# Performance work log

Measured on AMD Instinct MI355X. Metric: run time of the kernel, lower is better.

The kernel has to match this reference:

```python
import jax, jax.numpy as jnp
import numpy as np

H = 16      # num_attention_heads
D = 64      # head_dim
W = 256     # one-sided attention window (tokens attend to +/- W neighbors)


def setup_inputs() -> dict:
    key = jax.random.key(0)
    ks = jax.random.split(key, 7)
    B, S, E = 2, 4096, 1024
    init = lambda k, shape: jax.random.normal(k, shape, jnp.float32) * 0.02
    return {
        "hidden_states": jax.random.normal(ks[0], (B, S, E), jnp.float32),
        "Wq": init(ks[1], (E, E)), "bq": init(ks[2], (E,)),
        "Wk": init(ks[3], (E, E)), "bk": init(ks[4], (E,)),
        "Wv": init(ks[5], (E, E)), "bv": init(ks[6], (E,)),
    }


def _sliding_window_attn(q, k, v, S):
    """q,k,v: [B,H,S,D]. Banded attention: query i attends keys |i-j|<=W.
    Implemented via overlapping chunks (sliding_chunks style), never forming SxS."""
    B = q.shape[0]
    C = S // W  # number of query chunks
    qc = q.reshape(B, H, C, W, D)

    def window(x):
        # pad one chunk each side, then stack 3 consecutive chunks per query chunk
        xp = jnp.pad(x, ((0, 0), (0, 0), (W, W), (0, 0)))
        xr = xp.reshape(B, H, C + 2, W, D)
        return jnp.concatenate([xr[:, :, i:i + C] for i in range(3)], axis=3)  # [B,H,C,3W,D]

    kc, vc = window(k), window(v)

    i = jnp.arange(W)[:, None]            # query offset within chunk
    j = jnp.arange(3 * W)[None, :]        # key offset within 3W window
    band = jnp.abs(j - W - i) <= W        # [W,3W] band mask
    kpos = jnp.arange(C)[:, None, None] * W + (j - W)[None]  # absolute key pos [C,1,3W]
    valid = band[None] & (kpos >= 0) & (kpos < S)             # [C,W,3W]

    scores = jnp.einsum('bhcqd,bhckd->bhcqk', qc, kc)         # [B,H,C,W,3W]
    scores = jnp.where(valid[None, None], scores, -jnp.inf)
    probs = jax.nn.softmax(scores, axis=-1)
    out = jnp.einsum('bhcqk,bhckd->bhcqd', probs, vc)         # [B,H,C,W,D]
    return out.reshape(B, H, S, D)


def reference(hidden_states, Wq, bq, Wk, bk, Wv, bv):
    B, S, E = hidden_states.shape
    scale = 1.0 / np.sqrt(D).astype(np.float32)

    def split_heads(x):  # [B,S,E] -> [B,H,S,D]
        return x.reshape(B, S, H, D).transpose(0, 2, 1, 3)

    q = split_heads((hidden_states @ Wq.T + bq) * scale)
    k = split_heads(hidden_states @ Wk.T + bk)
    v = split_heads(hidden_states @ Wv.T + bv)

    ctx = _sliding_window_attn(q, k, v, S)                 # [B,H,S,D]
    return ctx.transpose(0, 2, 1, 3).reshape(B, S, E)      # [B,S,E]
```

## Files before the change

kernel.cpp:

```cpp
#include <hip/hip_runtime.h>

#define NH 16
#define HD 64
#define WIN 256
#define BB 2
#define SS 4096
#define EE 1024

typedef __attribute__((ext_vector_type(8))) short short8;
typedef __attribute__((ext_vector_type(4))) float floatx4;
typedef __attribute__((ext_vector_type(4))) unsigned short ushort4v;

__device__ inline unsigned short f2bf(float f) {
    unsigned u = __builtin_bit_cast(unsigned, f);
    u += 0x7fffu + ((u >> 16) & 1u);
    return (unsigned short)(u >> 16);
}

__global__ __launch_bounds__(256)
void cvt_kernel(const float* __restrict__ X,
                const float* __restrict__ W0,
                const float* __restrict__ W1,
                const float* __restrict__ W2,
                unsigned short* __restrict__ out)
{
    size_t idx = (size_t)blockIdx.x * 256 + threadIdx.x;
    const size_t X4 = 2097152, W4 = 262144;
    const float* src; unsigned short* dst; size_t off;
    if (idx < X4)                { src = X;  dst = out;            off = idx; }
    else if (idx < X4 + W4)      { src = W0; dst = out + 8388608;  off = idx - X4; }
    else if (idx < X4 + 2 * W4)  { src = W1; dst = out + 9437184;  off = idx - X4 - W4; }
    else                         { src = W2; dst = out + 10485760; off = idx - X4 - 2 * W4; }
    float4 v = ((const float4*)src)[off];
    ushort4 u;
    u.x = f2bf(v.x); u.y = f2bf(v.y); u.z = f2bf(v.z); u.w = f2bf(v.w);
    ((ushort4*)dst)[off] = u;
}

__global__ __launch_bounds__(256, 4)
void qkv_gemm4(const unsigned short* __restrict__ Xb,
               const unsigned short* __restrict__ WbAll,
               const float* __restrict__ b0,
               const float* __restrict__ b1,
               const float* __restrict__ b2,
               unsigned short* __restrict__ Qo,
               unsigned short* __restrict__ Ko,
               unsigned short* __restrict__ Vo)
{
    const int id = blockIdx.x;
    const int xcd = id & 7;
    const int rest = id >> 3;
    const int ytile = xcd + 8 * (rest & 7);
    const int nm = rest >> 3;
    const int ntile = nm & 7;
    const int mode = nm >> 3;

    const unsigned short* Wm = WbAll + (size_t)mode * 1048576;
    const float* bm = (mode == 0) ? b0 : (mode == 1) ? b1 : b2;
    unsigned short* outp = (mode == 0) ? Qo : (mode == 1) ? Ko : Vo;

    const int m0 = ytile * 128;
    const int n0 = ntile * 128;
    const int t = threadIdx.x;
    const int lane = t & 63;
    const int wv = t >> 6;
    const int wm = wv >> 1, wn = wv & 1;
    const int lg = lane >> 4, lc = lane & 15;

    __shared__ __attribute__((aligned(16))) unsigned short smem[16384];
    unsigned short* As[2] = { smem, smem + 4096 };
    unsigned short* Bs[2] = { smem + 8192, smem + 12288 };

    const int srow = lane >> 2;
    const int scol = (lane & 3) * 8;

    floatx4 acc[4][4];
#pragma unroll
    for (int i = 0; i < 4; ++i)
#pragma unroll
        for (int j = 0; j < 4; ++j)
            acc[i][j] = (floatx4)0.0f;

    for (int kt = 0; kt < EE; kt += 64) {
        if (kt) __syncthreads();
#pragma unroll
        for (int half = 0; half < 2; ++half) {
#pragma unroll
            for (int seg = 0; seg < 2; ++seg) {
                int r0 = wv * 32 + seg * 16;
                const unsigned short* asrc =
                    Xb + (size_t)(m0 + r0 + srow) * EE + kt + half * 32 + scol;
                const unsigned short* bsrc =
                    Wm + (size_t)(n0 + r0 + srow) * EE + kt + half * 32 + scol;
                __builtin_amdgcn_global_load_lds(
                    (const __attribute__((address_space(1))) unsigned int*)asrc,
                    (__attribute__((address_space(3))) unsigned int*)&As[half][r0 * 32], 16, 0, 0);
                __builtin_amdgcn_global_load_lds(
                    (const __attribute__((address_space(1))) unsigned int*)bsrc,
                    (__attribute__((address_space(3))) unsigned int*)&Bs[half][r0 * 32], 16, 0, 0);
            }
        }
        __syncthreads();

#pragma unroll
        for (int half = 0; half < 2; ++half) {
            short8 af[4], bfr[4];
#pragma unroll
            for (int mt = 0; mt < 4; ++mt)
                af[mt] = *(const short8*)(&As[half][(wm * 64 + mt * 16 + lc) * 32 + lg * 8]);
#pragma unroll
            for (int nt = 0; nt < 4; ++nt)
                bfr[nt] = *(const short8*)(&Bs[half][(wn * 64 + nt * 16 + lc) * 32 + lg * 8]);
#pragma unroll
            for (int mt = 0; mt < 4; ++mt)
#pragma unroll
                for (int nt = 0; nt < 4; ++nt)
                    acc[mt][nt] = __builtin_amdgcn_mfma_f32_16x16x32_bf16(
                        af[mt], bfr[nt], acc[mt][nt], 0, 0, 0);
        }
    }

    const int CST = 136;
    const float qscale = (mode == 0) ? 0.125f : 1.0f;
#pragma unroll
    for (int p = 0; p < 2; ++p) {
        __syncthreads();
        if (mode < 2) {
            if (wm == p) {
#pragma unroll
                for (int nt = 0; nt < 4; ++nt) {
                    float bias = bm[n0 + wn * 64 + nt * 16 + lc];
#pragma unroll
                    for (int mt = 0; mt < 4; ++mt)
#pragma unroll
                        for (int r = 0; r < 4; ++r) {
                            int ml = mt * 16 + lg * 4 + r;
                            int nl = wn * 64 + nt * 16 + lc;
                            smem[ml * CST + nl] = f2bf((acc[mt][nt][r] + bias) * qscale);
                        }
                }
            }
        } else {
            if (wn == p) {
#pragma unroll
                for (int nt = 0; nt < 4; ++nt) {
                    float bias = bm[n0 + p * 64 + nt * 16 + lc];
#pragma unroll
                    for (int mt = 0; mt < 4; ++mt) {
                        ushort4v pk;
#pragma unroll
                        for (int r = 0; r < 4; ++r)
                            pk[r] = f2bf(acc[mt][nt][r] + bias);
                        int nl = nt * 16 + lc;
                        int col = wm * 64 + mt * 16 + lg * 4;
                        *(ushort4v*)(&smem[nl * CST + col]) = pk;
                    }
                }
            }
        }
        __syncthreads();
#pragma unroll
        for (int q = 0; q < 4; ++q) {
            int c = q * 256 + t;
            int row = c >> 4;
            int j = c & 15;
            uint4 val = *(const uint4*)(&smem[row * CST + j * 8]);
            if (mode < 2) {
                int m = m0 + p * 64 + row;
                int bb = m >> 12, s = m & (SS - 1);
                int n = n0 + j * 8;
                int hh = n >> 6, dd = n & 63;
                *(uint4*)(outp + (((size_t)bb * NH + hh) * SS + s) * HD + dd) = val;
            } else {
                int n = n0 + p * 64 + row;
                int hh = n >> 6, dd = n & 63;
                int m = m0 + j * 8;
                int bb = m >> 12, s = m & (SS - 1);
                *(uint4*)(outp + (((size_t)bb * NH + hh) * HD + dd) * SS + s) = val;
            }
        }
    }
}

__global__ __launch_bounds__(256, 2)
void swa_kernel(const unsigned short* __restrict__ Qp_,
                const unsigned short* __restrict__ Kp_,
                const unsigned short* __restrict__ Vp_,
                float* __restrict__ outp)
{
    const int id = blockIdx.x;
    const int xcd = id & 7;
    const int idx = id >> 3;
    const int bh = xcd + 8 * (idx >> 5);
    const int q0 = (idx & 31) * 128;
    const int b = bh >> 4;
    const int h = bh & 15;
    const int t = threadIdx.x, lane = t & 63, wv = t >> 6;
    const int lg = lane >> 4, lc = lane & 15;
    const size_t bhs = (size_t)b * NH + h;
    const unsigned short* Qp = Qp_ + bhs * (size_t)SS * HD;
    const unsigned short* Kp = Kp_ + bhs * (size_t)SS * HD;
    const unsigned short* Vp = Vp_ + bhs * (size_t)HD * SS;
    const int qbase = q0 + wv * 32;

    short8 qf[2][2];
#pragma unroll
    for (int rt = 0; rt < 2; ++rt)
#pragma unroll
        for (int hh = 0; hh < 2; ++hh)
            qf[rt][hh] = *(const short8*)(Qp + (size_t)(qbase + rt * 16 + lc) * HD + hh * 32 + lg * 8);

    floatx4 o[2][4];
    float lsum[2][4];
#pragma unroll
    for (int rt = 0; rt < 2; ++rt)
#pragma unroll
        for (int i = 0; i < 4; ++i) { o[rt][i] = (floatx4)0.0f; lsum[rt][i] = 0.0f; }

    __shared__ __attribute__((aligned(16))) unsigned short kvs[2][2][4096];
    __shared__ __attribute__((aligned(16))) unsigned short Ps[4][2][16][72];

    const int kbeg = (q0 >= WIN) ? (q0 - WIN) : 0;
    const int kend = (q0 + 128 + WIN <= SS) ? (q0 + 128 + WIN) : SS;

    const int sr = lane >> 3;
    const int sj = lane & 7;
    const int swz = (sj ^ sr) * 8;

#define STAGE(buf, k0_)                                                              \
    {                                                                                \
        _Pragma("unroll")                                                            \
        for (int i = 0; i < 2; ++i) {                                                \
            int rbase = 16 * wv + i * 8;                                             \
            const unsigned short* ks = Kp + (size_t)((k0_) + rbase + sr) * HD + swz; \
            const unsigned short* vs = Vp + (size_t)(rbase + sr) * SS + (k0_) + swz; \
            __builtin_amdgcn_global_load_lds(                                        \
                (const __attribute__((address_space(1))) unsigned int*)ks,           \
                (__attribute__((address_space(3))) unsigned int*)&kvs[buf][0][rbase * 64], 16, 0, 0); \
            __builtin_amdgcn_global_load_lds(                                        \
                (const __attribute__((address_space(1))) unsigned int*)vs,           \
                (__attribute__((address_space(3))) unsigned int*)&kvs[buf][1][rbase * 64], 16, 0, 0); \
        }                                                                            \
    }

    STAGE(0, kbeg)

    int cur = 0;
    for (int k0 = kbeg; k0 < kend; k0 += 64, cur ^= 1) {
        __syncthreads();
        bool active = (k0 + 63 >= qbase - WIN) && (k0 <= qbase + 31 + WIN);
        short8 kc[4][2], vf[4][2];
        if (active) {
#pragma unroll
            for (int nt = 0; nt < 4; ++nt)
#pragma unroll
                for (int hh = 0; hh < 2; ++hh) {
                    int row = nt * 16 + lc;
                    kc[nt][hh] = *(const short8*)(&kvs[cur][0][row * 64 + (((hh * 4 + lg) ^ (row & 7)) * 8)]);
                    vf[nt][hh] = *(const short8*)(&kvs[cur][1][row * 64 + (((hh * 4 + lg) ^ (row & 7)) * 8)]);
                }
        }
        if (k0 + 64 < kend) STAGE(cur ^ 1, k0 + 64)
        if (!active) continue;

        bool fullband = (k0 >= qbase - 225) && (k0 <= qbase + 193);

        floatx4 sc[2][4];
#pragma unroll
        for (int rt = 0; rt < 2; ++rt)
#pragma unroll
            for (int nt = 0; nt < 4; ++nt) {
                floatx4 z = (floatx4)0.0f;
                z = __builtin_amdgcn_mfma_f32_16x16x32_bf16(qf[rt][0], kc[nt][0], z, 0, 0, 0);
                sc[rt][nt] = __builtin_amdgcn_mfma_f32_16x16x32_bf16(qf[rt][1], kc[nt][1], z, 0, 0, 0);
            }
#pragma unroll
        for (int rt = 0; rt < 2; ++rt)
#pragma unroll
            for (int nt = 0; nt < 4; ++nt)
#pragma unroll
                for (int r = 0; r < 4; ++r)
                    sc[rt][nt][r] = __expf(sc[rt][nt][r]);
        if (!fullband) {
#pragma unroll
            for (int rt = 0; rt < 2; ++rt)
#pragma unroll
                for (int nt = 0; nt < 4; ++nt) {
                    int kk = k0 + nt * 16 + lc;
#pragma unroll
                    for (int r = 0; r < 4; ++r) {
                        int dq = (qbase + rt * 16 + lg * 4 + r) - kk;
                        if (dq > WIN || dq < -WIN) sc[rt][nt][r] = 0.0f;
                    }
                }
        }
#pragma unroll
        for (int rt = 0; rt < 2; ++rt)
#pragma unroll
            for (int r = 0; r < 4; ++r)
                lsum[rt][r] += (sc[rt][0][r] + sc[rt][1][r]) + (sc[rt][2][r] + sc[rt][3][r]);
#pragma unroll
        for (int rt = 0; rt < 2; ++rt)
#pragma unroll
            for (int nt = 0; nt < 4; ++nt)
#pragma unroll
                for (int r = 0; r < 4; ++r)
                    Ps[wv][rt][lg * 4 + r][nt * 16 + lc] = f2bf(sc[rt][nt][r]);
#pragma unroll
        for (int rt = 0; rt < 2; ++rt) {
            short8 pa0 = *(const short8*)(&Ps[wv][rt][lc][lg * 8]);
            short8 pa1 = *(const short8*)(&Ps[wv][rt][lc][32 + lg * 8]);
#pragma unroll
            for (int nt2 = 0; nt2 < 4; ++nt2) {
                o[rt][nt2] = __builtin_amdgcn_mfma_f32_16x16x32_bf16(pa0, vf[nt2][0], o[rt][nt2], 0, 0, 0);
                o[rt][nt2] = __builtin_amdgcn_mfma_f32_16x16x32_bf16(pa1, vf[nt2][1], o[rt][nt2], 0, 0, 0);
            }
        }
    }

#pragma unroll
    for (int rt = 0; rt < 2; ++rt)
#pragma unroll
        for (int r = 0; r < 4; ++r) {
            float rs = lsum[rt][r];
#pragma unroll
            for (int off = 1; off < 16; off <<= 1)
                rs += __shfl_xor(rs, off, 64);
            lsum[rt][r] = 1.0f / rs;
        }
#pragma unroll
    for (int rt = 0; rt < 2; ++rt)
#pragma unroll
        for (int nt2 = 0; nt2 < 4; ++nt2)
#pragma unroll
            for (int r = 0; r < 4; ++r) {
                int q = qbase + rt * 16 + lg * 4 + r;
                int d = nt2 * 16 + lc;
                outp[((size_t)b * SS + q) * EE + h * HD + d] = o[rt][nt2][r] * lsum[rt][r];
            }
}

extern "C" void kernel_launch(void* const* d_in, const int* in_sizes, int n_in,
                              void* d_out, int out_size, void* d_ws, size_t ws_size,
                              hipStream_t stream) {
    const float* X  = (const float*)d_in[0];
    const float* Wq = (const float*)d_in[1];
    const float* bq = (const float*)d_in[2];
    const float* Wk = (const float*)d_in[3];
    const float* bk = (const float*)d_in[4];
    const float* Wv = (const float*)d_in[5];
    const float* bv = (const float*)d_in[6];

    const size_t qkv_elems = (size_t)BB * NH * SS * HD;
    unsigned short* Qw = (unsigned short*)d_ws;
    unsigned short* Kw = Qw + qkv_elems;
    unsigned short* Vw = Kw + qkv_elems;

    unsigned short* cvt = (unsigned short*)d_out;
    const unsigned short* Xb = cvt;
    const unsigned short* WbAll = cvt + 8388608;

    cvt_kernel<<<dim3(11264), 256, 0, stream>>>(X, Wq, Wk, Wv, cvt);
    qkv_gemm4<<<dim3(1536), 256, 0, stream>>>(
        Xb, WbAll, bq, bk, bv, Qw, Kw, Vw);
    swa_kernel<<<dim3(1024), 256, 0, stream>>>(Qw, Kw, Vw, (float*)d_out);
}
```

Baseline: 193.5 us.

## Split attention work across 8 waves of 16 query rows each

```diff
diff --git a/kernel.cpp b/kernel.cpp
--- a/kernel.cpp
+++ b/kernel.cpp
@@ -182,7 +182,7 @@
     }
 }
 
-__global__ __launch_bounds__(256, 2)
+__global__ __launch_bounds__(512, 4)
 void swa_kernel(const unsigned short* __restrict__ Qp_,
                 const unsigned short* __restrict__ Kp_,
                 const unsigned short* __restrict__ Vp_,
@@ -201,24 +201,20 @@
     const unsigned short* Qp = Qp_ + bhs * (size_t)SS * HD;
     const unsigned short* Kp = Kp_ + bhs * (size_t)SS * HD;
     const unsigned short* Vp = Vp_ + bhs * (size_t)HD * SS;
-    const int qbase = q0 + wv * 32;
-
-    short8 qf[2][2];
-#pragma unroll
-    for (int rt = 0; rt < 2; ++rt)
-#pragma unroll
-        for (int hh = 0; hh < 2; ++hh)
-            qf[rt][hh] = *(const short8*)(Qp + (size_t)(qbase + rt * 16 + lc) * HD + hh * 32 + lg * 8);
-
-    floatx4 o[2][4];
-    float lsum[2][4];
-#pragma unroll
-    for (int rt = 0; rt < 2; ++rt)
-#pragma unroll
-        for (int i = 0; i < 4; ++i) { o[rt][i] = (floatx4)0.0f; lsum[rt][i] = 0.0f; }
+    const int qbase = q0 + wv * 16;
+
+    short8 qf[2];
+#pragma unroll
+    for (int hh = 0; hh < 2; ++hh)
+        qf[hh] = *(const short8*)(Qp + (size_t)(qbase + lc) * HD + hh * 32 + lg * 8);
+
+    floatx4 o[4];
+    float lsum[4];
+#pragma unroll
+    for (int i = 0; i < 4; ++i) { o[i] = (floatx4)0.0f; lsum[i] = 0.0f; }
 
     __shared__ __attribute__((aligned(16))) unsigned short kvs[2][2][4096];
-    __shared__ __attribute__((aligned(16))) unsigned short Ps[4][2][16][72];
+    __shared__ __attribute__((aligned(16))) unsigned short Ps[8][16][72];
 
     const int kbeg = (q0 >= WIN) ? (q0 - WIN) : 0;
     const int kend = (q0 + 128 + WIN <= SS) ? (q0 + 128 + WIN) : SS;
@@ -229,18 +225,15 @@
 
 #define STAGE(buf, k0_)                                                              \
     {                                                                                \
-        _Pragma("unroll")                                                            \
-        for (int i = 0; i < 2; ++i) {                                                \
-            int rbase = 16 * wv + i * 8;                                             \
-            const unsigned short* ks = Kp + (size_t)((k0_) + rbase + sr) * HD + swz; \
-            const unsigned short* vs = Vp + (size_t)(rbase + sr) * SS + (k0_) + swz; \
-            __builtin_amdgcn_global_load_lds(                                        \
-                (const __attribute__((address_space(1))) unsigned int*)ks,           \
-                (__attribute__((address_space(3))) unsigned int*)&kvs[buf][0][rbase * 64], 16, 0, 0); \
-            __builtin_amdgcn_global_load_lds(                                        \
-                (const __attribute__((address_space(1))) unsigned int*)vs,           \
-                (__attribute__((address_space(3))) unsigned int*)&kvs[buf][1][rbase * 64], 16, 0, 0); \
-        }                                                                            \
+        const int rbase = 8 * wv;                                                    \
+        const unsigned short* ks = Kp + (size_t)((k0_) + rbase + sr) * HD + swz;     \
+        const unsigned short* vs = Vp + (size_t)(rbase + sr) * SS + (k0_) + swz;     \
+        __builtin_amdgcn_global_load_lds(                                            \
+            (const __attribute__((address_space(1))) unsigned int*)ks,               \
+            (__attribute__((address_space(3))) unsigned int*)&kvs[buf][0][rbase * 64], 16, 0, 0); \
+        __builtin_amdgcn_global_load_lds(                                            \
+            (const __attribute__((address_space(1))) unsigned int*)vs,               \
+            (__attribute__((address_space(3))) unsigned int*)&kvs[buf][1][rbase * 64], 16, 0, 0); \
     }
 
     STAGE(0, kbeg)
@@ -248,8 +241,8 @@
     int cur = 0;
     for (int k0 = kbeg; k0 < kend; k0 += 64, cur ^= 1) {
         __syncthreads();
-        bool active = (k0 + 63 >= qbase - WIN) && (k0 <= qbase + 31 + WIN);
-        short8 kc[4][2], vf[4][2];
+        bool active = (k0 + 63 >= qbase - WIN) && (k0 <= qbase + 15 + WIN);
+        short8 kc[4][2];
         if (active) {
 #pragma unroll
             for (int nt = 0; nt < 4; ++nt)
@@ -257,87 +250,73 @@
                 for (int hh = 0; hh < 2; ++hh) {
                     int row = nt * 16 + lc;
                     kc[nt][hh] = *(const short8*)(&kvs[cur][0][row * 64 + (((hh * 4 + lg) ^ (row & 7)) * 8)]);
-                    vf[nt][hh] = *(const short8*)(&kvs[cur][1][row * 64 + (((hh * 4 + lg) ^ (row & 7)) * 8)]);
                 }
         }
         if (k0 + 64 < kend) STAGE(cur ^ 1, k0 + 64)
         if (!active) continue;
 
-        bool fullband = (k0 >= qbase - 225) && (k0 <= qbase + 193);
-
-        floatx4 sc[2][4];
-#pragma unroll
-        for (int rt = 0; rt < 2; ++rt)
+        bool fullband = (k0 >= qbase - 241) && (k0 <= qbase + 193);
+
+        floatx4 sc[4];
+#pragma unroll
+        for (int nt = 0; nt < 4; ++nt) {
+            floatx4 z = (floatx4)0.0f;
+            z = __builtin_amdgcn_mfma_f32_16x16x32_bf16(qf[0], kc[nt][0], z, 0, 0, 0);
+            sc[nt] = __builtin_amdgcn_mfma_f32_16x16x32_bf16(qf[1], kc[nt][1], z, 0, 0, 0);
+        }
+#pragma unroll
+        for (int nt = 0; nt < 4; ++nt)
+#pragma unroll
+            for (int r = 0; r < 4; ++r)
+                sc[nt][r] = __expf(sc[nt][r]);
+        if (!fullband) {
 #pragma unroll
             for (int nt = 0; nt < 4; ++nt) {
-                floatx4 z = (floatx4)0.0f;
-                z = __builtin_amdgcn_mfma_f32_16x16x32_bf16(qf[rt][0], kc[nt][0], z, 0, 0, 0);
-                sc[rt][nt] = __builtin_amdgcn_mfma_f32_16x16x32_bf16(qf[rt][1], kc[nt][1], z, 0, 0, 0);
-            }
-#pragma unroll
-        for (int rt = 0; rt < 2; ++rt)
-#pragma unroll
-            for (int nt = 0; nt < 4; ++nt)
-#pragma unroll
-                for (int r = 0; r < 4; ++r)
-                    sc[rt][nt][r] = __expf(sc[rt][nt][r]);
-        if (!fullband) {
-#pragma unroll
-            for (int rt = 0; rt < 2; ++rt)
-#pragma unroll
-                for (int nt = 0; nt < 4; ++nt) {
-                    int kk = k0 + nt * 16 + lc;
-#pragma unroll
-                    for (int r = 0; r < 4; ++r) {
-                        int dq = (qbase + rt * 16 + lg * 4 + r) - kk;
-                        if (dq > WIN || dq < -WIN) sc[rt][nt][r] = 0.0f;
-                    }
+                int kk = k0 + nt * 16 + lc;
+#pragma unroll
+                for (int r = 0; r < 4; ++r) {
+                    int dq = (qbase + lg * 4 + r) - kk;
+                    if (dq > WIN || dq < -WIN) sc[nt][r] = 0.0f;
                 }
-        }
-#pragma unroll
-        for (int rt = 0; rt < 2; ++rt)
+            }
+        }
+#pragma unroll
+        for (int r = 0; r < 4; ++r)
+            lsum[r] += (sc[0][r] + sc[1][r]) + (sc[2][r] + sc[3][r]);
+#pragma unroll
+        for (int nt = 0; nt < 4; ++nt)
 #pragma unroll
             for (int r = 0; r < 4; ++r)
-                lsum[rt][r] += (sc[rt][0][r] + sc[rt][1][r]) + (sc[rt][2][r] + sc[rt][3][r]);
-#pragma unroll
-        for (int rt = 0; rt < 2; ++rt)
-#pragma unroll
-            for (int nt = 0; nt < 4; ++nt)
-#pragma unroll
-                for (int r = 0; r < 4; ++r)
-                    Ps[wv][rt][lg * 4 + r][nt * 16 + lc] = f2bf(sc[rt][nt][r]);
-#pragma unroll
-        for (int rt = 0; rt < 2; ++rt) {
-            short8 pa0 = *(const short8*)(&Ps[wv][rt][lc][lg * 8]);
-            short8 pa1 = *(const short8*)(&Ps[wv][rt][lc][32 + lg * 8]);
-#pragma unroll
-            for (int nt2 = 0; nt2 < 4; ++nt2) {
-                o[rt][nt2] = __builtin_amdgcn_mfma_f32_16x16x32_bf16(pa0, vf[nt2][0], o[rt][nt2], 0, 0, 0);
-                o[rt][nt2] = __builtin_amdgcn_mfma_f32_16x16x32_bf16(pa1, vf[nt2][1], o[rt][nt2], 0, 0, 0);
-            }
-        }
-    }
-
-#pragma unroll
-    for (int rt = 0; rt < 2; ++rt)
+                Ps[wv][lg * 4 + r][nt * 16 + lc] = f2bf(sc[nt][r]);
+
+        short8 pa0 = *(const short8*)(&Ps[wv][lc][lg * 8]);
+        short8 pa1 = *(const short8*)(&Ps[wv][lc][32 + lg * 8]);
+#pragma unroll
+        for (int nt2 = 0; nt2 < 4; ++nt2) {
+            int row = nt2 * 16 + lc;
+            short8 vf0 = *(const short8*)(&kvs[cur][1][row * 64 + (((0 + lg) ^ (row & 7)) * 8)]);
+            short8 vf1 = *(const short8*)(&kvs[cur][1][row * 64 + (((4 + lg) ^ (row & 7)) * 8)]);
+            o[nt2] = __builtin_amdgcn_mfma_f32_16x16x32_bf16(pa0, vf0, o[nt2], 0, 0, 0);
+            o[nt2] = __builtin_amdgcn_mfma_f32_16x16x32_bf16(pa1, vf1, o[nt2], 0, 0, 0);
+        }
+    }
+
+#pragma unroll
+    for (int r = 0; r < 4; ++r) {
+        float rs = lsum[r];
+#pragma unroll
+        for (int off = 1; off < 16; off <<= 1)
+            rs += __shfl_xor(rs, off, 64);
+        lsum[r] = 1.0f / rs;
+    }
+#pragma unroll
+    for (int nt2 = 0; nt2 < 4; ++nt2)
 #pragma unroll
         for (int r = 0; r < 4; ++r) {
-            float rs = lsum[rt][r];
-#pragma unroll
-            for (int off = 1; off < 16; off <<= 1)
-                rs += __shfl_xor(rs, off, 64);
-            lsum[rt][r] = 1.0f / rs;
-        }
-#pragma unroll
-    for (int rt = 0; rt < 2; ++rt)
-#pragma unroll
-        for (int nt2 = 0; nt2 < 4; ++nt2)
-#pragma unroll
-            for (int r = 0; r < 4; ++r) {
-                int q = qbase + rt * 16 + lg * 4 + r;
-                int d = nt2 * 16 + lc;
-                outp[((size_t)b * SS + q) * EE + h * HD + d] = o[rt][nt2][r] * lsum[rt][r];
-            }
+            int q = qbase + lg * 4 + r;
+            int d = nt2 * 16 + lc;
+            outp[((size_t)b * SS + q) * EE + h * HD + d] = o[nt2][r] * lsum[r];
+        }
 }
 
 extern "C" void kernel_launch(void* const* d_in, const int* in_sizes, int n_in,
@@ -363,5 +342,5 @@
     cvt_kernel<<<dim3(11264), 256, 0, stream>>>(X, Wq, Wk, Wv, cvt);
     qkv_gemm4<<<dim3(1536), 256, 0, stream>>>(
         Xb, WbAll, bq, bk, bv, Qw, Kw, Vw);
-    swa_kernel<<<dim3(1024), 256, 0, stream>>>(Qw, Kw, Vw, (float*)d_out);
-}
+    swa_kernel<<<dim3(1024), 512, 0, stream>>>(Qw, Kw, Vw, (float*)d_out);
+}
```

New measurement: 192.5 us. About the same (-0.6%).

## Switch attention to 32x32 MFMA with transposed scores and register-resident P

Applied to the files above, without the earlier changes.

```diff
diff --git a/kernel.cpp b/kernel.cpp
--- a/kernel.cpp
+++ b/kernel.cpp
@@ -9,7 +9,9 @@
 
 typedef __attribute__((ext_vector_type(8))) short short8;
 typedef __attribute__((ext_vector_type(4))) float floatx4;
+typedef __attribute__((ext_vector_type(16))) float floatx16;
 typedef __attribute__((ext_vector_type(4))) unsigned short ushort4v;
+typedef __attribute__((ext_vector_type(4))) unsigned int uint4v;
 
 __device__ inline unsigned short f2bf(float f) {
     unsigned u = __builtin_bit_cast(unsigned, f);
@@ -182,7 +184,7 @@
     }
 }
 
-__global__ __launch_bounds__(256, 2)
+__global__ __launch_bounds__(256, 4)
 void swa_kernel(const unsigned short* __restrict__ Qp_,
                 const unsigned short* __restrict__ Kp_,
                 const unsigned short* __restrict__ Vp_,
@@ -196,29 +198,24 @@
     const int b = bh >> 4;
     const int h = bh & 15;
     const int t = threadIdx.x, lane = t & 63, wv = t >> 6;
-    const int lg = lane >> 4, lc = lane & 15;
+    const int l31 = lane & 31, hf = lane >> 5;
     const size_t bhs = (size_t)b * NH + h;
     const unsigned short* Qp = Qp_ + bhs * (size_t)SS * HD;
     const unsigned short* Kp = Kp_ + bhs * (size_t)SS * HD;
     const unsigned short* Vp = Vp_ + bhs * (size_t)HD * SS;
     const int qbase = q0 + wv * 32;
 
-    short8 qf[2][2];
-#pragma unroll
-    for (int rt = 0; rt < 2; ++rt)
-#pragma unroll
-        for (int hh = 0; hh < 2; ++hh)
-            qf[rt][hh] = *(const short8*)(Qp + (size_t)(qbase + rt * 16 + lc) * HD + hh * 32 + lg * 8);
-
-    floatx4 o[2][4];
-    float lsum[2][4];
-#pragma unroll
-    for (int rt = 0; rt < 2; ++rt)
-#pragma unroll
-        for (int i = 0; i < 4; ++i) { o[rt][i] = (floatx4)0.0f; lsum[rt][i] = 0.0f; }
+    short8 qf[4];
+#pragma unroll
+    for (int dc = 0; dc < 4; ++dc)
+        qf[dc] = *(const short8*)(Qp + (size_t)(qbase + l31) * HD + dc * 16 + hf * 8);
+
+    floatx16 o0 = (floatx16)0.0f;
+    floatx16 o1 = (floatx16)0.0f;
+    float lsq = 0.0f;
 
     __shared__ __attribute__((aligned(16))) unsigned short kvs[2][2][4096];
-    __shared__ __attribute__((aligned(16))) unsigned short Ps[4][2][16][72];
+    __shared__ float lsums[4][32];
 
     const int kbeg = (q0 >= WIN) ? (q0 - WIN) : 0;
     const int kend = (q0 + 128 + WIN <= SS) ? (q0 + 128 + WIN) : SS;
@@ -248,96 +245,86 @@
     int cur = 0;
     for (int k0 = kbeg; k0 < kend; k0 += 64, cur ^= 1) {
         __syncthreads();
+        if (k0 + 64 < kend) STAGE(cur ^ 1, k0 + 64)
         bool active = (k0 + 63 >= qbase - WIN) && (k0 <= qbase + 31 + WIN);
-        short8 kc[4][2], vf[4][2];
-        if (active) {
-#pragma unroll
-            for (int nt = 0; nt < 4; ++nt)
-#pragma unroll
-                for (int hh = 0; hh < 2; ++hh) {
-                    int row = nt * 16 + lc;
-                    kc[nt][hh] = *(const short8*)(&kvs[cur][0][row * 64 + (((hh * 4 + lg) ^ (row & 7)) * 8)]);
-                    vf[nt][hh] = *(const short8*)(&kvs[cur][1][row * 64 + (((hh * 4 + lg) ^ (row & 7)) * 8)]);
+        if (!active) continue;
+        bool fullband = (k0 >= qbase - 225) && (k0 <= qbase + 193);
+
+#pragma unroll
+        for (int ks = 0; ks < 2; ++ks) {
+            short8 kc[4];
+#pragma unroll
+            for (int dc = 0; dc < 4; ++dc) {
+                int row = ks * 32 + l31;
+                kc[dc] = *(const short8*)(&kvs[cur][0][row * 64 + (((dc * 2 + hf) ^ (row & 7)) * 8)]);
+            }
+            floatx16 z = (floatx16)0.0f;
+            z = __builtin_amdgcn_mfma_f32_32x32x16_bf16(kc[0], qf[0], z, 0, 0, 0);
+            z = __builtin_amdgcn_mfma_f32_32x32x16_bf16(kc[1], qf[1], z, 0, 0, 0);
+            z = __builtin_amdgcn_mfma_f32_32x32x16_bf16(kc[2], qf[2], z, 0, 0, 0);
+            z = __builtin_amdgcn_mfma_f32_32x32x16_bf16(kc[3], qf[3], z, 0, 0, 0);
+
+            float p[16];
+#pragma unroll
+            for (int r = 0; r < 16; ++r)
+                p[r] = __expf(z[r]);
+            if (!fullband) {
+#pragma unroll
+                for (int r = 0; r < 16; ++r) {
+                    int kk = k0 + ks * 32 + (r & 3) + 8 * (r >> 2) + 4 * hf;
+                    int dq = (qbase + l31) - kk;
+                    if (dq > WIN || dq < -WIN) p[r] = 0.0f;
                 }
-        }
-        if (k0 + 64 < kend) STAGE(cur ^ 1, k0 + 64)
-        if (!active) continue;
-
-        bool fullband = (k0 >= qbase - 225) && (k0 <= qbase + 193);
-
-        floatx4 sc[2][4];
-#pragma unroll
-        for (int rt = 0; rt < 2; ++rt)
-#pragma unroll
-            for (int nt = 0; nt < 4; ++nt) {
-                floatx4 z = (floatx4)0.0f;
-                z = __builtin_amdgcn_mfma_f32_16x16x32_bf16(qf[rt][0], kc[nt][0], z, 0, 0, 0);
-                sc[rt][nt] = __builtin_amdgcn_mfma_f32_16x16x32_bf16(qf[rt][1], kc[nt][1], z, 0, 0, 0);
-            }
-#pragma unroll
-        for (int rt = 0; rt < 2; ++rt)
-#pragma unroll
-            for (int nt = 0; nt < 4; ++nt)
-#pragma unroll
-                for (int r = 0; r < 4; ++r)
-                    sc[rt][nt][r] = __expf(sc[rt][nt][r]);
-        if (!fullband) {
-#pragma unroll
-            for (int rt = 0; rt < 2; ++rt)
-#pragma unroll
-                for (int nt = 0; nt < 4; ++nt) {
-                    int kk = k0 + nt * 16 + lc;
-#pragma unroll
-                    for (int r = 0; r < 4; ++r) {
-                        int dq = (qbase + rt * 16 + lg * 4 + r) - kk;
-                        if (dq > WIN || dq < -WIN) sc[rt][nt][r] = 0.0f;
-                    }
-                }
-        }
-#pragma unroll
-        for (int rt = 0; rt < 2; ++rt)
-#pragma unroll
-            for (int r = 0; r < 4; ++r)
-                lsum[rt][r] += (sc[rt][0][r] + sc[rt][1][r]) + (sc[rt][2][r] + sc[rt][3][r]);
-#pragma unroll
-        for (int rt = 0; rt < 2; ++rt)
-#pragma unroll
-            for (int nt = 0; nt < 4; ++nt)
-#pragma unroll
-                for (int r = 0; r < 4; ++r)
-                    Ps[wv][rt][lg * 4 + r][nt * 16 + lc] = f2bf(sc[rt][nt][r]);
-#pragma unroll
-        for (int rt = 0; rt < 2; ++rt) {
-            short8 pa0 = *(const short8*)(&Ps[wv][rt][lc][lg * 8]);
-            short8 pa1 = *(const short8*)(&Ps[wv][rt][lc][32 + lg * 8]);
-#pragma unroll
-            for (int nt2 = 0; nt2 < 4; ++nt2) {
-                o[rt][nt2] = __builtin_amdgcn_mfma_f32_16x16x32_bf16(pa0, vf[nt2][0], o[rt][nt2], 0, 0, 0);
-                o[rt][nt2] = __builtin_amdgcn_mfma_f32_16x16x32_bf16(pa1, vf[nt2][1], o[rt][nt2], 0, 0, 0);
-            }
-        }
-    }
-
-#pragma unroll
-    for (int rt = 0; rt < 2; ++rt)
-#pragma unroll
-        for (int r = 0; r < 4; ++r) {
-            float rs = lsum[rt][r];
-#pragma unroll
-            for (int off = 1; off < 16; off <<= 1)
-                rs += __shfl_xor(rs, off, 64);
-            lsum[rt][r] = 1.0f / rs;
-        }
-#pragma unroll
-    for (int rt = 0; rt < 2; ++rt)
-#pragma unroll
-        for (int nt2 = 0; nt2 < 4; ++nt2)
-#pragma unroll
-            for (int r = 0; r < 4; ++r) {
-                int q = qbase + rt * 16 + lg * 4 + r;
-                int d = nt2 * 16 + lc;
-                outp[((size_t)b * SS + q) * EE + h * HD + d] = o[rt][nt2][r] * lsum[rt][r];
-            }
+            }
+#pragma unroll
+            for (int r = 0; r < 16; ++r)
+                lsq += p[r];
+
+            unsigned int j0, j1, j2, j3, j4, j5, j6, j7;
+            asm("v_cvt_pk_bf16_f32 %0, %1, %2" : "=v"(j0) : "v"(p[0]),  "v"(p[1]));
+            asm("v_cvt_pk_bf16_f32 %0, %1, %2" : "=v"(j1) : "v"(p[2]),  "v"(p[3]));
+            asm("v_cvt_pk_bf16_f32 %0, %1, %2" : "=v"(j2) : "v"(p[4]),  "v"(p[5]));
+            asm("v_cvt_pk_bf16_f32 %0, %1, %2" : "=v"(j3) : "v"(p[6]),  "v"(p[7]));
+            asm("v_cvt_pk_bf16_f32 %0, %1, %2" : "=v"(j4) : "v"(p[8]),  "v"(p[9]));
+            asm("v_cvt_pk_bf16_f32 %0, %1, %2" : "=v"(j5) : "v"(p[10]), "v"(p[11]));
+            asm("v_cvt_pk_bf16_f32 %0, %1, %2" : "=v"(j6) : "v"(p[12]), "v"(p[13]));
+            asm("v_cvt_pk_bf16_f32 %0, %1, %2" : "=v"(j7) : "v"(p[14]), "v"(p[15]));
+            asm("v_permlane32_swap_b32 %0, %1" : "+v"(j0), "+v"(j2));
+            asm("v_permlane32_swap_b32 %0, %1" : "+v"(j1), "+v"(j3));
+            asm("v_permlane32_swap_b32 %0, %1" : "+v"(j4), "+v"(j6));
+            asm("v_permlane32_swap_b32 %0, %1" : "+v"(j5), "+v"(j7));
+            short8 pa0 = __builtin_bit_cast(short8, (uint4v){j0, j1, j2, j3});
+            short8 pa1 = __builtin_bit_cast(short8, (uint4v){j4, j5, j6, j7});
+
+            {
+                int row = l31;
+                short8 vf0 = *(const short8*)(&kvs[cur][1][row * 64 + (((ks * 4 + 0 + hf) ^ (row & 7)) * 8)]);
+                short8 vf1 = *(const short8*)(&kvs[cur][1][row * 64 + (((ks * 4 + 2 + hf) ^ (row & 7)) * 8)]);
+                o0 = __builtin_amdgcn_mfma_f32_32x32x16_bf16(pa0, vf0, o0, 0, 0, 0);
+                o0 = __builtin_amdgcn_mfma_f32_32x32x16_bf16(pa1, vf1, o0, 0, 0, 0);
+            }
+            {
+                int row = 32 + l31;
+                short8 vf0 = *(const short8*)(&kvs[cur][1][row * 64 + (((ks * 4 + 0 + hf) ^ (row & 7)) * 8)]);
+                short8 vf1 = *(const short8*)(&kvs[cur][1][row * 64 + (((ks * 4 + 2 + hf) ^ (row & 7)) * 8)]);
+                o1 = __builtin_amdgcn_mfma_f32_32x32x16_bf16(pa0, vf0, o1, 0, 0, 0);
+                o1 = __builtin_amdgcn_mfma_f32_32x32x16_bf16(pa1, vf1, o1, 0, 0, 0);
+            }
+        }
+    }
+
+    float tot = lsq + __shfl_xor(lsq, 32, 64);
+    if (lane < 32) lsums[wv][l31] = 1.0f / tot;
+
+#pragma unroll
+    for (int r = 0; r < 16; ++r) {
+        int qloc = (r & 3) + 8 * (r >> 2) + 4 * hf;
+        float inv = lsums[wv][qloc];
+        int q = qbase + qloc;
+        float* orow = outp + ((size_t)b * SS + q) * EE + h * HD;
+        orow[l31] = o0[r] * inv;
+        orow[32 + l31] = o1[r] * inv;
+    }
 }
 
 extern "C" void kernel_launch(void* const* d_in, const int* in_sizes, int n_in,
```

Measured after the change: 187.5 us. 3.1% less time.
